# Performance work log

Hardware: AMD Instinct MI355X
Metric: run time of the kernel (lower is better)

Reference implementation:

```python
import jax, jax.numpy as jnp
import numpy as np

EPS = 1e-6

def setup_inputs() -> dict:
    key = jax.random.key(0)
    k1, k2, k3 = jax.random.split(key, 3)
    B, C, H, W = 8, 384, 32, 32
    dim = C
    x = jax.random.normal(k1, (B, C, H, W), dtype=jnp.float32)
    # torch Linear weights: [out_features, in_features]
    w_qkv = jax.random.normal(k2, (3 * dim, dim), dtype=jnp.float32) * (dim ** -0.5)
    w_proj = jax.random.normal(k3, (dim, dim), dtype=jnp.float32) * (dim ** -0.5)
    ln_w = jnp.ones((dim,), dtype=jnp.float32)
    ln_b = jnp.zeros((dim,), dtype=jnp.float32)
    return {"x": x, "w_qkv": w_qkv, "w_proj": w_proj, "ln_w": ln_w, "ln_b": ln_b}

def reference(x, w_qkv, w_proj, ln_w, ln_b):
    num_heads = 8
    B, C, H, W = x.shape
    N = H * W
    head_dim = C // num_heads
    scale = head_dim ** -0.5

    tokens = jnp.transpose(x, (0, 2, 3, 1)).reshape(B, N, C)  # [B,N,C]
    residual = tokens
    # LayerNorm over last dim
    mu = jnp.mean(tokens, axis=-1, keepdims=True)
    var = jnp.mean(jnp.square(tokens - mu), axis=-1, keepdims=True)
    t = (tokens - mu) * jax.lax.rsqrt(var + EPS) * ln_w + ln_b

    qkv = t @ w_qkv.T                                  # [B,N,3C]
    qkv = qkv.reshape(B, N, 3, num_heads, head_dim)
    qkv = jnp.transpose(qkv, (2, 0, 3, 1, 4))          # [3,B,h,N,d]
    q, k, v = qkv[0], qkv[1], qkv[2]

    attn = jnp.einsum('bhnd,bhmd->bhnm', q, k) * scale  # [B,h,N,N]
    attn = jax.nn.softmax(attn, axis=-1)
    out = jnp.einsum('bhnm,bhmd->bhnd', attn, v)        # [B,h,N,d]
    out = jnp.transpose(out, (0, 2, 1, 3)).reshape(B, N, C)
    out = out @ w_proj.T
    out = residual + out
    return jnp.transpose(out.reshape(B, H, W, C), (0, 3, 1, 2))
```

## Files before the change

kernel.cpp:

```cpp
#include <hip/hip_runtime.h>
#include <math.h>

typedef __attribute__((ext_vector_type(4))) float f32x4;
typedef __attribute__((ext_vector_type(8))) short s16x8;

constexpr int B_ = 8, C_ = 384, N_ = 1024, NH_ = 8, D_ = 48;
constexpr float SCALE_ = 0.14433756729740643f;
constexpr float LOG2E_ = 1.4426950408889634f;
constexpr float EXP_BIAS_ = 8.0f * LOG2E_;

__device__ __forceinline__ unsigned short f2bf(float f) {
    unsigned u = __builtin_bit_cast(unsigned, f);
    u += 0x7fff + ((u >> 16) & 1);
    return (unsigned short)(u >> 16);
}
__device__ __forceinline__ unsigned short f2bf_trunc(float f) {
    return (unsigned short)(__builtin_bit_cast(unsigned, f) >> 16);
}
__device__ __forceinline__ float fexp2(float x) {
#if __has_builtin(__builtin_amdgcn_exp2f)
    return __builtin_amdgcn_exp2f(x);
#else
    return exp2f(x);
#endif
}

__global__ __launch_bounds__(256) void ln_cvt_kernel(const float* __restrict__ x,
                                                     const float* __restrict__ lnw,
                                                     const float* __restrict__ lnb,
                                                     const float* __restrict__ wq,
                                                     const float* __restrict__ wp,
                                                     unsigned short* __restrict__ t,
                                                     unsigned short* __restrict__ wqb,
                                                     unsigned short* __restrict__ wpb) {
    int tid = threadIdx.x;
    int gid = blockIdx.x * 256 + tid;
    for (int i = gid; i < 1152 * 384; i += 512 * 256) wqb[i] = f2bf(wq[i]);
    for (int i = gid; i < 384 * 384;  i += 512 * 256) wpb[i] = f2bf(wp[i]);

    __shared__ float xs[384][17];
    __shared__ float wgt[384], bia[384];
    int b  = blockIdx.x >> 6;
    int n0 = (blockIdx.x & 63) << 4;
    for (int i = tid; i < 384; i += 256) { wgt[i] = lnw[i]; bia[i] = lnb[i]; }

    const float* xb = x + (size_t)b * 384 * 1024;
    #pragma unroll
    for (int k = 0; k < 6; k++) {
        int f = tid + k * 256;
        int c = f >> 2, li = (f & 3) * 4;
        float4 v = *(const float4*)&xb[(size_t)c * 1024 + n0 + li];
        xs[c][li] = v.x; xs[c][li + 1] = v.y; xs[c][li + 2] = v.z; xs[c][li + 3] = v.w;
    }
    __syncthreads();

    int l = tid >> 4, part = tid & 15;
    float s = 0.f, sq = 0.f;
    #pragma unroll
    for (int j = 0; j < 24; j++) {
        float v = xs[part + j * 16][l];
        s += v; sq += v * v;
    }
    #pragma unroll
    for (int off = 1; off <= 8; off <<= 1) {
        s  += __shfl_xor(s,  off);
        sq += __shfl_xor(sq, off);
    }
    float mu   = s * (1.0f / 384.0f);
    float rstd = rsqrtf(sq * (1.0f / 384.0f) - mu * mu + 1e-6f);

    unsigned short* tp = t + (size_t)(b * 1024 + n0 + l) * 384 + part * 24;
    unsigned o32[12];
    #pragma unroll
    for (int m = 0; m < 12; m++) {
        int c0 = part * 24 + m * 2;
        unsigned lo = f2bf((xs[c0][l]     - mu) * rstd * wgt[c0]     + bia[c0]);
        unsigned hi = f2bf((xs[c0 + 1][l] - mu) * rstd * wgt[c0 + 1] + bia[c0 + 1]);
        o32[m] = lo | (hi << 16);
    }
    #pragma unroll
    for (int m = 0; m < 3; m++) {
        int4 pk = { (int)o32[m * 4], (int)o32[m * 4 + 1], (int)o32[m * 4 + 2], (int)o32[m * 4 + 3] };
        *(int4*)&tp[m * 8] = pk;
    }
}

__global__ __launch_bounds__(256) void qkv_mfma(const unsigned short* __restrict__ t,
                                                const unsigned short* __restrict__ w,
                                                unsigned short* __restrict__ qn,
                                                unsigned short* __restrict__ kn,
                                                unsigned short* __restrict__ vt) {
    __shared__ __align__(16) unsigned short lds[128 * 72 * 2];
    unsigned short (*As)[72]  = (unsigned short (*)[72])&lds[0];
    unsigned short (*Bs)[72]  = (unsigned short (*)[72])&lds[128 * 72];
    unsigned short (*Cs)[136] = (unsigned short (*)[136])&lds[0];

    int tid = threadIdx.x;
    int m0 = blockIdx.x * 128;
    int jb = blockIdx.y;
    int j0 = jb * 128;
    int lane = tid & 63, wid = tid >> 6;
    int wr = wid >> 1, wc = wid & 1;
    int q16 = lane & 15, quad = lane >> 4;

    f32x4 acc[4][4] = {};

    const int srow = tid >> 1, sc = (tid & 1) * 32;
    for (int k0 = 0; k0 < 384; k0 += 64) {
        const unsigned short* ga = &t[(size_t)(m0 + srow) * 384 + k0 + sc];
        const unsigned short* gb = &w[(size_t)(j0 + srow) * 384 + k0 + sc];
        *(int4*)&As[srow][sc]      = *(const int4*)(ga);
        *(int4*)&As[srow][sc + 8]  = *(const int4*)(ga + 8);
        *(int4*)&As[srow][sc + 16] = *(const int4*)(ga + 16);
        *(int4*)&As[srow][sc + 24] = *(const int4*)(ga + 24);
        *(int4*)&Bs[srow][sc]      = *(const int4*)(gb);
        *(int4*)&Bs[srow][sc + 8]  = *(const int4*)(gb + 8);
        *(int4*)&Bs[srow][sc + 16] = *(const int4*)(gb + 16);
        *(int4*)&Bs[srow][sc + 24] = *(const int4*)(gb + 24);
        __syncthreads();
        #pragma unroll
        for (int s = 0; s < 2; s++) {
            s16x8 af[4], bfr[4];
            #pragma unroll
            for (int mi = 0; mi < 4; mi++) af[mi]  = *(const s16x8*)&As[wr * 64 + mi * 16 + q16][s * 32 + quad * 8];
            #pragma unroll
            for (int ni = 0; ni < 4; ni++) bfr[ni] = *(const s16x8*)&Bs[wc * 64 + ni * 16 + q16][s * 32 + quad * 8];
            #pragma unroll
            for (int mi = 0; mi < 4; mi++)
                #pragma unroll
                for (int ni = 0; ni < 4; ni++)
                    acc[mi][ni] = __builtin_amdgcn_mfma_f32_16x16x32_bf16(af[mi], bfr[ni], acc[mi][ni], 0, 0, 0);
        }
        __syncthreads();
    }

    if (jb < 6) {
        const float sc0 = (jb < 3) ? SCALE_ * LOG2E_ : 1.0f;
        unsigned short* dst = (jb < 3) ? qn : kn;
        int coff = (jb < 3 ? jb : jb - 3) * 128;
        #pragma unroll
        for (int mi = 0; mi < 4; mi++)
            #pragma unroll
            for (int ni = 0; ni < 4; ni++)
                #pragma unroll
                for (int r = 0; r < 4; r++)
                    Cs[wr * 64 + mi * 16 + quad * 4 + r][wc * 64 + ni * 16 + q16] = f2bf(acc[mi][ni][r] * sc0);
        __syncthreads();
        #pragma unroll
        for (int i = tid; i < 2048; i += 256) {
            int rr = i >> 4, cc = (i & 15) * 8;
            int m = m0 + rr;
            int bsel = m >> 10, nn = m & 1023;
            *(int4*)&dst[(size_t)(bsel * 1024 + nn) * 384 + coff + cc] = *(const int4*)&Cs[rr][cc];
        }
    } else {
        #pragma unroll
        for (int mi = 0; mi < 4; mi++) {
            int m_base = m0 + wr * 64 + mi * 16 + quad * 4;
            int bb = m_base >> 10;
            int nn = m_base & 1023;
            #pragma unroll
            for (int ni = 0; ni < 4; ni++) {
                int c2 = (jb - 6) * 128 + wc * 64 + ni * 16 + q16;
                int head = c2 / 48;
                int dd = c2 - head * 48;
                f32x4 a = acc[mi][ni];
                size_t base = (((size_t)bb * 8 + head) * 48 + dd) * 1024 + nn;
                ushort4 v4 = { f2bf(a.x), f2bf(a.y), f2bf(a.z), f2bf(a.w) };
                *(ushort4*)&vt[base] = v4;
            }
        }
    }
}

__global__ __launch_bounds__(256) void attn_mfma(const unsigned short* __restrict__ qn,
                                                 const unsigned short* __restrict__ kn,
                                                 const unsigned short* __restrict__ vt,
                                                 unsigned short* __restrict__ ao) {
    __shared__ __align__(16) unsigned short Ks[2][64][72];
    __shared__ __align__(16) unsigned short Vt[2][48][72];
    __shared__ __align__(16) unsigned short Ps[4][16][72];

    unsigned short (*Kflat)[72] = (unsigned short (*)[72])&Ks[0][0][0];

    int tid = threadIdx.x, lane = tid & 63, wid = tid >> 6;
    int q16 = lane & 15, quad = lane >> 4;
    int qt = blockIdx.x, h = blockIdx.y, b = blockIdx.z;
    const unsigned short* qp = qn + (size_t)b * 1024 * 384 + h * 48;
    const unsigned short* kp = kn + (size_t)b * 1024 * 384 + h * 48;
    const unsigned short* vp = vt + ((size_t)b * NH_ + h) * 48 * N_;

    int4 z4 = {0, 0, 0, 0};

    {
        int r = tid >> 1, off = (tid & 1) * 24;
        const unsigned short* gp = qp + (size_t)(qt * 128 + r) * 384 + off;
        *(int4*)&Kflat[r][off]      = *(const int4*)gp;
        *(int4*)&Kflat[r][off + 8]  = *(const int4*)(gp + 8);
        *(int4*)&Kflat[r][off + 16] = *(const int4*)(gp + 16);
        if ((tid & 1) == 0) { *(int4*)&Kflat[r][48] = z4; *(int4*)&Kflat[r][56] = z4; }
    }
    __syncthreads();

    s16x8 qf[2][2];
    #pragma unroll
    for (int g = 0; g < 2; g++) {
        qf[g][0] = *(const s16x8*)&Kflat[wid * 32 + g * 16 + q16][quad * 8];
        qf[g][1] = *(const s16x8*)&Kflat[wid * 32 + g * 16 + q16][32 + quad * 8];
    }
    __syncthreads();

    const int kr = tid >> 1, koff = (tid & 1) * 24;
    const int vi = tid - 128;

    {
        if (tid < 128) {
            const unsigned short* gp = kp + (size_t)kr * 384 + koff;
            *(int4*)&Ks[0][kr][koff]      = *(const int4*)gp;
            *(int4*)&Ks[0][kr][koff + 8]  = *(const int4*)(gp + 8);
            *(int4*)&Ks[0][kr][koff + 16] = *(const int4*)(gp + 16);
            if ((tid & 1) == 0) { *(int4*)&Ks[0][kr][48] = z4; *(int4*)&Ks[0][kr][56] = z4; }
        } else {
            #pragma unroll
            for (int j = 0; j < 3; j++) {
                int c = vi + j * 128;
                int row = c >> 3, g8 = (c & 7) * 8;
                *(int4*)&Vt[0][row][g8] = *(const int4*)&vp[(size_t)row * 1024 + g8];
            }
        }
    }
    __syncthreads();

    f32x4 o[2][3] = {};
    f32x4 lrv[2] = {};

    for (int kt = 0; kt < 16; kt++) {
        int cur = kt & 1;

        int4 pf0, pf1, pf2;
        if (kt < 15) {
            if (tid < 128) {
                const unsigned short* gp = kp + (size_t)((kt + 1) * 64 + kr) * 384 + koff;
                pf0 = *(const int4*)gp;
                pf1 = *(const int4*)(gp + 8);
                pf2 = *(const int4*)(gp + 16);
            } else {
                pf0 = *(const int4*)&vp[(size_t)((vi +   0) >> 3) * 1024 + (kt + 1) * 64 + ((vi +   0) & 7) * 8];
                pf1 = *(const int4*)&vp[(size_t)((vi + 128) >> 3) * 1024 + (kt + 1) * 64 + ((vi + 128) & 7) * 8];
                pf2 = *(const int4*)&vp[(size_t)((vi + 256) >> 3) * 1024 + (kt + 1) * 64 + ((vi + 256) & 7) * 8];
            }
        }

        f32x4 s[2][4];
        __builtin_amdgcn_s_setprio(1);
        #pragma unroll
        for (int nt = 0; nt < 4; nt++) {
            s16x8 k0 = *(const s16x8*)&Ks[cur][nt * 16 + q16][quad * 8];
            s16x8 k1 = *(const s16x8*)&Ks[cur][nt * 16 + q16][32 + quad * 8];
            #pragma unroll
            for (int g = 0; g < 2; g++) {
                f32x4 z = {};
                z = __builtin_amdgcn_mfma_f32_16x16x32_bf16(qf[g][0], k0, z, 0, 0, 0);
                z = __builtin_amdgcn_mfma_f32_16x16x32_bf16(qf[g][1], k1, z, 0, 0, 0);
                s[g][nt] = z;
            }
        }
        __builtin_amdgcn_s_setprio(0);

        s16x8 vf[2][3];
        #pragma unroll
        for (int c = 0; c < 2; c++)
            #pragma unroll
            for (int dt = 0; dt < 3; dt++)
                vf[c][dt] = *(const s16x8*)&Vt[cur][dt * 16 + q16][c * 32 + quad * 8];

        #pragma unroll
        for (int g = 0; g < 2; g++) {
            #pragma unroll
            for (int nt = 0; nt < 4; nt++) {
                s[g][nt].x = fexp2(s[g][nt].x - EXP_BIAS_);
                s[g][nt].y = fexp2(s[g][nt].y - EXP_BIAS_);
                s[g][nt].z = fexp2(s[g][nt].z - EXP_BIAS_);
                s[g][nt].w = fexp2(s[g][nt].w - EXP_BIAS_);
                lrv[g] += s[g][nt];
            }
            #pragma unroll
            for (int nt = 0; nt < 4; nt++)
                #pragma unroll
                for (int r = 0; r < 4; r++)
                    Ps[wid][quad * 4 + r][nt * 16 + q16] = f2bf_trunc(s[g][nt][r]);
            __builtin_amdgcn_s_setprio(1);
            #pragma unroll
            for (int c = 0; c < 2; c++) {
                s16x8 pfr = *(const s16x8*)&Ps[wid][q16][c * 32 + quad * 8];
                #pragma unroll
                for (int dt = 0; dt < 3; dt++)
                    o[g][dt] = __builtin_amdgcn_mfma_f32_16x16x32_bf16(pfr, vf[c][dt], o[g][dt], 0, 0, 0);
            }
            __builtin_amdgcn_s_setprio(0);
        }

        if (kt < 15) {
            int nb = cur ^ 1;
            if (tid < 128) {
                *(int4*)&Ks[nb][kr][koff]      = pf0;
                *(int4*)&Ks[nb][kr][koff + 8]  = pf1;
                *(int4*)&Ks[nb][kr][koff + 16] = pf2;
                if ((tid & 1) == 0) { *(int4*)&Ks[nb][kr][48] = z4; *(int4*)&Ks[nb][kr][56] = z4; }
            } else {
                *(int4*)&Vt[nb][(vi +   0) >> 3][((vi +   0) & 7) * 8] = pf0;
                *(int4*)&Vt[nb][(vi + 128) >> 3][((vi + 128) & 7) * 8] = pf1;
                *(int4*)&Vt[nb][(vi + 256) >> 3][((vi + 256) & 7) * 8] = pf2;
            }
        }
        __syncthreads();
    }

    #pragma unroll
    for (int g = 0; g < 2; g++) {
        #pragma unroll
        for (int off = 1; off <= 8; off <<= 1) {
            lrv[g].x += __shfl_xor(lrv[g].x, off);
            lrv[g].y += __shfl_xor(lrv[g].y, off);
            lrv[g].z += __shfl_xor(lrv[g].z, off);
            lrv[g].w += __shfl_xor(lrv[g].w, off);
        }
    }

    #pragma unroll
    for (int g = 0; g < 2; g++) {
        f32x4 inv;
        inv.x = __builtin_amdgcn_rcpf(lrv[g].x);
        inv.y = __builtin_amdgcn_rcpf(lrv[g].y);
        inv.z = __builtin_amdgcn_rcpf(lrv[g].z);
        inv.w = __builtin_amdgcn_rcpf(lrv[g].w);
        #pragma unroll
        for (int dt = 0; dt < 3; dt++)
            #pragma unroll
            for (int r = 0; r < 4; r++)
                Kflat[wid * 32 + g * 16 + quad * 4 + r][dt * 16 + q16] = f2bf(o[g][dt][r] * inv[r]);
    }
    __syncthreads();

    {
        int r = tid >> 1, off = (tid & 1) * 24;
        unsigned short* dst = ao + ((size_t)b * 1024 + qt * 128 + r) * 384 + h * 48 + off;
        *(int4*)dst        = *(const int4*)&Kflat[r][off];
        *(int4*)(dst + 8)  = *(const int4*)&Kflat[r][off + 8];
        *(int4*)(dst + 16) = *(const int4*)&Kflat[r][off + 16];
    }
}

__global__ __launch_bounds__(256) void proj_mfma(const unsigned short* __restrict__ ao,
                                                 const unsigned short* __restrict__ w,
                                                 const float* __restrict__ x,
                                                 float* __restrict__ out) {
    __shared__ __align__(16) unsigned short As[64][72];
    __shared__ __align__(16) unsigned short Bs[64][72];

    int tid = threadIdx.x;
    int m0 = blockIdx.x * 64;
    int j0 = blockIdx.y * 64;
    int lane = tid & 63, wid = tid >> 6;
    int wr = wid >> 1, wc = wid & 1;
    int q16 = lane & 15, quad = lane >> 4;

    f32x4 acc[2][2] = {};

    const int srow = tid >> 2, sc = (tid & 3) * 16;
    for (int k0 = 0; k0 < 384; k0 += 64) {
        const unsigned short* ga = &ao[(size_t)(m0 + srow) * 384 + k0 + sc];
        const unsigned short* gb = &w[(size_t)(j0 + srow) * 384 + k0 + sc];
        *(int4*)&As[srow][sc]     = *(const int4*)(ga);
        *(int4*)&As[srow][sc + 8] = *(const int4*)(ga + 8);
        *(int4*)&Bs[srow][sc]     = *(const int4*)(gb);
        *(int4*)&Bs[srow][sc + 8] = *(const int4*)(gb + 8);
        __syncthreads();
        #pragma unroll
        for (int s = 0; s < 2; s++) {
            s16x8 af[2], bfr[2];
            #pragma unroll
            for (int mi = 0; mi < 2; mi++) af[mi]  = *(const s16x8*)&As[wr * 32 + mi * 16 + q16][s * 32 + quad * 8];
            #pragma unroll
            for (int ni = 0; ni < 2; ni++) bfr[ni] = *(const s16x8*)&Bs[wc * 32 + ni * 16 + q16][s * 32 + quad * 8];
            #pragma unroll
            for (int mi = 0; mi < 2; mi++)
                #pragma unroll
                for (int ni = 0; ni < 2; ni++)
                    acc[mi][ni] = __builtin_amdgcn_mfma_f32_16x16x32_bf16(af[mi], bfr[ni], acc[mi][ni], 0, 0, 0);
        }
        __syncthreads();
    }

    #pragma unroll
    for (int mi = 0; mi < 2; mi++) {
        int m_base = m0 + wr * 32 + mi * 16 + quad * 4;
        int bb = m_base >> 10;
        int nn = m_base & 1023;
        #pragma unroll
        for (int ni = 0; ni < 2; ni++) {
            int col = j0 + wc * 32 + ni * 16 + q16;
            size_t idx = ((size_t)bb * 384 + col) * 1024 + nn;
            float4 xr = *(const float4*)&x[idx];
            f32x4 a = acc[mi][ni];
            float4 ov = { xr.x + a.x, xr.y + a.y, xr.z + a.z, xr.w + a.w };
            *(float4*)&out[idx] = ov;
        }
    }
}

extern "C" void kernel_launch(void* const* d_in, const int* in_sizes, int n_in,
                              void* d_out, int out_size, void* d_ws, size_t ws_size,
                              hipStream_t stream) {
    const float* x     = (const float*)d_in[0];
    const float* wqkv  = (const float*)d_in[1];
    const float* wproj = (const float*)d_in[2];
    const float* lnw   = (const float*)d_in[3];
    const float* lnb   = (const float*)d_in[4];
    float* out = (float*)d_out;

    unsigned short* ws16 = (unsigned short*)d_ws;
    size_t off = 0;
    unsigned short* t_bf  = ws16 + off; off += (size_t)8192 * 384;
    unsigned short* wq_bf = ws16 + off; off += (size_t)1152 * 384;
    unsigned short* wp_bf = ws16 + off; off += (size_t)384 * 384;
    unsigned short* qn    = ws16 + off; off += (size_t)8192 * 384;
    unsigned short* kn    = ws16 + off; off += (size_t)8192 * 384;
    unsigned short* vt    = ws16 + off; off += (size_t)64 * 48 * 1024;
    unsigned short* ao_bf = ws16 + off; off += (size_t)8192 * 384;

    ln_cvt_kernel<<<512, 256, 0, stream>>>(x, lnw, lnb, wqkv, wproj, t_bf, wq_bf, wp_bf);
    qkv_mfma<<<dim3(64, 9), 256, 0, stream>>>(t_bf, wq_bf, qn, kn, vt);
    attn_mfma<<<dim3(8, NH_, B_), 256, 0, stream>>>(qn, kn, vt, ao_bf);
    proj_mfma<<<dim3(128, 6), 256, 0, stream>>>(ao_bf, wp_bf, x, out);
}
```

Measured before the change: 136.1 us.

## Use 128-key tiles and transposed MFMA operands in attention kernel

The attention kernel now stages 128 keys per iteration (8 iterations instead of 16), with all threads loading both K and V instead of splitting the work, halving the number of barriers. The MFMA operand order is swapped so scores come out transposed. Each lane then holds one query row, which lets P be written with packed bf16 conversion (v_cvt_pk_bf16_f32) in 8-byte stores and cuts the row-sum reduction to two shuffles. It uses more LDS per block, which may lower occupancy, and P is now rounded rather than truncated.

```diff
diff --git a/kernel.cpp b/kernel.cpp
--- a/kernel.cpp
+++ b/kernel.cpp
@@ -13,9 +13,6 @@
     unsigned u = __builtin_bit_cast(unsigned, f);
     u += 0x7fff + ((u >> 16) & 1);
     return (unsigned short)(u >> 16);
-}
-__device__ __forceinline__ unsigned short f2bf_trunc(float f) {
-    return (unsigned short)(__builtin_bit_cast(unsigned, f) >> 16);
 }
 __device__ __forceinline__ float fexp2(float x) {
 #if __has_builtin(__builtin_amdgcn_exp2f)
@@ -23,6 +20,11 @@
 #else
     return exp2f(x);
 #endif
+}
+__device__ __forceinline__ unsigned pk_bf16(float a, float b) {
+    unsigned r;
+    asm("v_cvt_pk_bf16_f32 %0, %1, %2" : "=v"(r) : "v"(a), "v"(b));
+    return r;
 }
 
 __global__ __launch_bounds__(256) void ln_cvt_kernel(const float* __restrict__ x,
@@ -177,8 +179,8 @@
                                                  const unsigned short* __restrict__ kn,
                                                  const unsigned short* __restrict__ vt,
                                                  unsigned short* __restrict__ ao) {
-    __shared__ __align__(16) unsigned short Ks[2][64][72];
-    __shared__ __align__(16) unsigned short Vt[2][48][72];
+    __shared__ __align__(16) unsigned short Ks[2][128][72];
+    __shared__ __align__(16) unsigned short Vt[2][48][136];
     __shared__ __align__(16) unsigned short Ps[4][16][72];
 
     unsigned short (*Kflat)[72] = (unsigned short (*)[72])&Ks[0][0][0];
@@ -208,137 +210,128 @@
         qf[g][0] = *(const s16x8*)&Kflat[wid * 32 + g * 16 + q16][quad * 8];
         qf[g][1] = *(const s16x8*)&Kflat[wid * 32 + g * 16 + q16][32 + quad * 8];
     }
+    *(int4*)&Ks[1][tid >> 1][48 + (tid & 1) * 8] = z4;
     __syncthreads();
 
     const int kr = tid >> 1, koff = (tid & 1) * 24;
-    const int vi = tid - 128;
+    const int vr0 = tid >> 4, vc0 = (tid & 15) * 8;
 
     {
-        if (tid < 128) {
-            const unsigned short* gp = kp + (size_t)kr * 384 + koff;
-            *(int4*)&Ks[0][kr][koff]      = *(const int4*)gp;
-            *(int4*)&Ks[0][kr][koff + 8]  = *(const int4*)(gp + 8);
-            *(int4*)&Ks[0][kr][koff + 16] = *(const int4*)(gp + 16);
-            if ((tid & 1) == 0) { *(int4*)&Ks[0][kr][48] = z4; *(int4*)&Ks[0][kr][56] = z4; }
-        } else {
-            #pragma unroll
-            for (int j = 0; j < 3; j++) {
-                int c = vi + j * 128;
-                int row = c >> 3, g8 = (c & 7) * 8;
-                *(int4*)&Vt[0][row][g8] = *(const int4*)&vp[(size_t)row * 1024 + g8];
-            }
-        }
+        const unsigned short* gp = kp + (size_t)kr * 384 + koff;
+        *(int4*)&Ks[0][kr][koff]      = *(const int4*)gp;
+        *(int4*)&Ks[0][kr][koff + 8]  = *(const int4*)(gp + 8);
+        *(int4*)&Ks[0][kr][koff + 16] = *(const int4*)(gp + 16);
+        *(int4*)&Vt[0][vr0][vc0]      = *(const int4*)&vp[(size_t)vr0 * 1024 + vc0];
+        *(int4*)&Vt[0][vr0 + 16][vc0] = *(const int4*)&vp[(size_t)(vr0 + 16) * 1024 + vc0];
+        *(int4*)&Vt[0][vr0 + 32][vc0] = *(const int4*)&vp[(size_t)(vr0 + 32) * 1024 + vc0];
     }
     __syncthreads();
 
     f32x4 o[2][3] = {};
-    f32x4 lrv[2] = {};
-
-    for (int kt = 0; kt < 16; kt++) {
+    float lr[2] = {0.f, 0.f};
+
+    for (int kt = 0; kt < 8; kt++) {
         int cur = kt & 1;
 
-        int4 pf0, pf1, pf2;
-        if (kt < 15) {
-            if (tid < 128) {
-                const unsigned short* gp = kp + (size_t)((kt + 1) * 64 + kr) * 384 + koff;
-                pf0 = *(const int4*)gp;
-                pf1 = *(const int4*)(gp + 8);
-                pf2 = *(const int4*)(gp + 16);
-            } else {
-                pf0 = *(const int4*)&vp[(size_t)((vi +   0) >> 3) * 1024 + (kt + 1) * 64 + ((vi +   0) & 7) * 8];
-                pf1 = *(const int4*)&vp[(size_t)((vi + 128) >> 3) * 1024 + (kt + 1) * 64 + ((vi + 128) & 7) * 8];
-                pf2 = *(const int4*)&vp[(size_t)((vi + 256) >> 3) * 1024 + (kt + 1) * 64 + ((vi + 256) & 7) * 8];
-            }
-        }
-
-        f32x4 s[2][4];
-        __builtin_amdgcn_s_setprio(1);
-        #pragma unroll
-        for (int nt = 0; nt < 4; nt++) {
-            s16x8 k0 = *(const s16x8*)&Ks[cur][nt * 16 + q16][quad * 8];
-            s16x8 k1 = *(const s16x8*)&Ks[cur][nt * 16 + q16][32 + quad * 8];
-            #pragma unroll
-            for (int g = 0; g < 2; g++) {
-                f32x4 z = {};
-                z = __builtin_amdgcn_mfma_f32_16x16x32_bf16(qf[g][0], k0, z, 0, 0, 0);
-                z = __builtin_amdgcn_mfma_f32_16x16x32_bf16(qf[g][1], k1, z, 0, 0, 0);
-                s[g][nt] = z;
-            }
-        }
-        __builtin_amdgcn_s_setprio(0);
-
-        s16x8 vf[2][3];
-        #pragma unroll
-        for (int c = 0; c < 2; c++)
-            #pragma unroll
-            for (int dt = 0; dt < 3; dt++)
-                vf[c][dt] = *(const s16x8*)&Vt[cur][dt * 16 + q16][c * 32 + quad * 8];
-
-        #pragma unroll
-        for (int g = 0; g < 2; g++) {
-            #pragma unroll
-            for (int nt = 0; nt < 4; nt++) {
-                s[g][nt].x = fexp2(s[g][nt].x - EXP_BIAS_);
-                s[g][nt].y = fexp2(s[g][nt].y - EXP_BIAS_);
-                s[g][nt].z = fexp2(s[g][nt].z - EXP_BIAS_);
-                s[g][nt].w = fexp2(s[g][nt].w - EXP_BIAS_);
-                lrv[g] += s[g][nt];
-            }
-            #pragma unroll
-            for (int nt = 0; nt < 4; nt++)
-                #pragma unroll
-                for (int r = 0; r < 4; r++)
-                    Ps[wid][quad * 4 + r][nt * 16 + q16] = f2bf_trunc(s[g][nt][r]);
+        int4 kpf0, kpf1, kpf2, vpf0, vpf1, vpf2;
+        if (kt < 7) {
+            const unsigned short* gp = kp + (size_t)((kt + 1) * 128 + kr) * 384 + koff;
+            kpf0 = *(const int4*)gp;
+            kpf1 = *(const int4*)(gp + 8);
+            kpf2 = *(const int4*)(gp + 16);
+            int nb0 = (kt + 1) * 128;
+            vpf0 = *(const int4*)&vp[(size_t)vr0 * 1024 + nb0 + vc0];
+            vpf1 = *(const int4*)&vp[(size_t)(vr0 + 16) * 1024 + nb0 + vc0];
+            vpf2 = *(const int4*)&vp[(size_t)(vr0 + 32) * 1024 + nb0 + vc0];
+        }
+
+        #pragma unroll
+        for (int hh = 0; hh < 2; hh++) {
+            f32x4 s[2][4];
             __builtin_amdgcn_s_setprio(1);
             #pragma unroll
-            for (int c = 0; c < 2; c++) {
-                s16x8 pfr = *(const s16x8*)&Ps[wid][q16][c * 32 + quad * 8];
-                #pragma unroll
-                for (int dt = 0; dt < 3; dt++)
-                    o[g][dt] = __builtin_amdgcn_mfma_f32_16x16x32_bf16(pfr, vf[c][dt], o[g][dt], 0, 0, 0);
+            for (int nt4 = 0; nt4 < 4; nt4++) {
+                int ntg = hh * 4 + nt4;
+                s16x8 k0 = *(const s16x8*)&Ks[cur][ntg * 16 + q16][quad * 8];
+                s16x8 k1 = *(const s16x8*)&Ks[cur][ntg * 16 + q16][32 + quad * 8];
+                #pragma unroll
+                for (int g = 0; g < 2; g++) {
+                    f32x4 z = {};
+                    z = __builtin_amdgcn_mfma_f32_16x16x32_bf16(k0, qf[g][0], z, 0, 0, 0);
+                    z = __builtin_amdgcn_mfma_f32_16x16x32_bf16(k1, qf[g][1], z, 0, 0, 0);
+                    s[g][nt4] = z;
+                }
             }
             __builtin_amdgcn_s_setprio(0);
-        }
-
-        if (kt < 15) {
+
+            #pragma unroll
+            for (int g = 0; g < 2; g++)
+                #pragma unroll
+                for (int nt4 = 0; nt4 < 4; nt4++) {
+                    s[g][nt4].x = fexp2(s[g][nt4].x - EXP_BIAS_);
+                    s[g][nt4].y = fexp2(s[g][nt4].y - EXP_BIAS_);
+                    s[g][nt4].z = fexp2(s[g][nt4].z - EXP_BIAS_);
+                    s[g][nt4].w = fexp2(s[g][nt4].w - EXP_BIAS_);
+                    lr[g] += (s[g][nt4].x + s[g][nt4].y) + (s[g][nt4].z + s[g][nt4].w);
+                }
+
+            s16x8 vf[2][3];
+            #pragma unroll
+            for (int c2 = 0; c2 < 2; c2++)
+                #pragma unroll
+                for (int dt = 0; dt < 3; dt++)
+                    vf[c2][dt] = *(const s16x8*)&Vt[cur][dt * 16 + q16][(2 * hh + c2) * 32 + quad * 8];
+
+            #pragma unroll
+            for (int g = 0; g < 2; g++) {
+                #pragma unroll
+                for (int n2 = 0; n2 < 4; n2++) {
+                    unsigned lo = pk_bf16(s[g][n2].x, s[g][n2].y);
+                    unsigned hi = pk_bf16(s[g][n2].z, s[g][n2].w);
+                    uint2 pkw = { lo, hi };
+                    *(uint2*)&Ps[wid][q16][n2 * 16 + quad * 4] = pkw;
+                }
+                #pragma unroll
+                for (int c2 = 0; c2 < 2; c2++) {
+                    s16x8 pfr = *(const s16x8*)&Ps[wid][q16][c2 * 32 + quad * 8];
+                    __builtin_amdgcn_s_setprio(1);
+                    #pragma unroll
+                    for (int dt = 0; dt < 3; dt++)
+                        o[g][dt] = __builtin_amdgcn_mfma_f32_16x16x32_bf16(vf[c2][dt], pfr, o[g][dt], 0, 0, 0);
+                    __builtin_amdgcn_s_setprio(0);
+                }
+            }
+        }
+
+        if (kt < 7) {
             int nb = cur ^ 1;
-            if (tid < 128) {
-                *(int4*)&Ks[nb][kr][koff]      = pf0;
-                *(int4*)&Ks[nb][kr][koff + 8]  = pf1;
-                *(int4*)&Ks[nb][kr][koff + 16] = pf2;
-                if ((tid & 1) == 0) { *(int4*)&Ks[nb][kr][48] = z4; *(int4*)&Ks[nb][kr][56] = z4; }
-            } else {
-                *(int4*)&Vt[nb][(vi +   0) >> 3][((vi +   0) & 7) * 8] = pf0;
-                *(int4*)&Vt[nb][(vi + 128) >> 3][((vi + 128) & 7) * 8] = pf1;
-                *(int4*)&Vt[nb][(vi + 256) >> 3][((vi + 256) & 7) * 8] = pf2;
-            }
+            *(int4*)&Ks[nb][kr][koff]      = kpf0;
+            *(int4*)&Ks[nb][kr][koff + 8]  = kpf1;
+            *(int4*)&Ks[nb][kr][koff + 16] = kpf2;
+            *(int4*)&Vt[nb][vr0][vc0]      = vpf0;
+            *(int4*)&Vt[nb][vr0 + 16][vc0] = vpf1;
+            *(int4*)&Vt[nb][vr0 + 32][vc0] = vpf2;
         }
         __syncthreads();
     }
 
     #pragma unroll
     for (int g = 0; g < 2; g++) {
-        #pragma unroll
-        for (int off = 1; off <= 8; off <<= 1) {
-            lrv[g].x += __shfl_xor(lrv[g].x, off);
-            lrv[g].y += __shfl_xor(lrv[g].y, off);
-            lrv[g].z += __shfl_xor(lrv[g].z, off);
-            lrv[g].w += __shfl_xor(lrv[g].w, off);
-        }
+        lr[g] += __shfl_xor(lr[g], 16);
+        lr[g] += __shfl_xor(lr[g], 32);
     }
 
     #pragma unroll
     for (int g = 0; g < 2; g++) {
-        f32x4 inv;
-        inv.x = __builtin_amdgcn_rcpf(lrv[g].x);
-        inv.y = __builtin_amdgcn_rcpf(lrv[g].y);
-        inv.z = __builtin_amdgcn_rcpf(lrv[g].z);
-        inv.w = __builtin_amdgcn_rcpf(lrv[g].w);
-        #pragma unroll
-        for (int dt = 0; dt < 3; dt++)
-            #pragma unroll
-            for (int r = 0; r < 4; r++)
-                Kflat[wid * 32 + g * 16 + quad * 4 + r][dt * 16 + q16] = f2bf(o[g][dt][r] * inv[r]);
+        float inv = __builtin_amdgcn_rcpf(lr[g]);
+        #pragma unroll
+        for (int dt = 0; dt < 3; dt++) {
+            f32x4 a = o[g][dt];
+            unsigned u0 = (unsigned)f2bf(a.x * inv) | ((unsigned)f2bf(a.y * inv) << 16);
+            unsigned u1 = (unsigned)f2bf(a.z * inv) | ((unsigned)f2bf(a.w * inv) << 16);
+            uint2 pkw = { u0, u1 };
+            *(uint2*)&Kflat[wid * 32 + g * 16 + q16][dt * 16 + quad * 4] = pkw;
+        }
     }
     __syncthreads();
 
```

Result: no change. 137.4 us (+0.9%).
